# Optimization experiments

Hardware: AMD Instinct MI355X
Metric: run time of the kernel (lower is better)

Reference implementation:

```python
import jax, jax.numpy as jnp
import numpy as np

ALPHA = 1.0
BETA = 1.0
GAMMA = 1.0
WEIGHT_LOSS = 1.0
EPS_DENOM = 1e-20


def setup_inputs() -> dict:
    key = jax.random.key(0)
    k1, k2 = jax.random.split(key)
    B, P, C = 128, 256, 1000
    classification_head_weight = jax.random.normal(k1, (C, P), dtype=jnp.float32)
    similarity_score = jax.random.uniform(k2, (B, P), dtype=jnp.float32)
    return {
        "classification_head_weight": classification_head_weight,
        "similarity_score": similarity_score,
    }


def reference(classification_head_weight, similarity_score):
    # importance[b, p, c] = similarity_score[b, p] * classification_head_weight[c, p]
    imp = jnp.einsum('bp,cp->bpc', similarity_score, classification_head_weight)
    B, P, C = imp.shape
    imp_sq = imp * imp

    # norm over p (dim=1) -> [B, C]; sum over c -> [B]
    norm_over_p = jnp.sqrt(jnp.sum(imp_sq, axis=1))      # [B, C]
    term_a = jnp.sum(norm_over_p, axis=1) ** 2           # [B]
    # norm over c (dim=2) -> [B, P]; sum over p -> [B]
    norm_over_c = jnp.sqrt(jnp.sum(imp_sq, axis=2))      # [B, P]
    term_b = jnp.sum(norm_over_c, axis=1) ** 2           # [B]
    # frobenius norm over (p, c) per batch
    fro_sq = jnp.sum(imp_sq, axis=(1, 2))                # [B]
    fro = jnp.sqrt(fro_sq)                               # [B]

    sparsity = (ALPHA * term_a + BETA * term_b) / (fro_sq + EPS_DENOM)
    sparsity = sparsity / (P * C) ** 0.5
    sparsity = sparsity + GAMMA * fro
    loss = jnp.mean(sparsity)
    return WEIGHT_LOSS * loss
```

## Files before the change

### kernel.cpp

```cpp
#include <hip/hip_runtime.h>
#include <math.h>

#define BB 128
#define PP 256
#define CC 1000

#define NMAIN 504
#define NPREP 16
#define NCT   63

#define OFF_W  0
#define OFF_SQ 4096

__global__ __launch_bounds__(256) void k_one(const float* __restrict__ W,
                                             const float* __restrict__ S,
                                             float* __restrict__ wsf,
                                             float* __restrict__ out) {
    int bid = blockIdx.x;
    int t = threadIdx.x;

    if (bid < NMAIN) {
        __shared__ float s2s[16][260];
        __shared__ float red_sq[16][17];

        int bt = bid & 7;
        int ct = bid >> 3;
        int b0 = bt * 16;
        int c0 = ct * 16;

#pragma unroll
        for (int i = 0; i < 16; ++i) {
            int idx = t + 256 * i;
            int row = idx >> 8, col = idx & 255;
            float s = S[(b0 + row) * PP + col];
            s2s[row][col] = s * s;
        }
        __syncthreads();

        int bl = t & 15;
        int cl = t >> 4;
        int c = c0 + cl;

        float acc = 0.f;
        if (c < CC) {
            const float4* w4 = (const float4*)(W + c * PP);
#pragma unroll 4
            for (int p = 0; p < 64; ++p) {
                float4 w = w4[p];
                float4 s2 = *(const float4*)&s2s[bl][p * 4];
                acc += s2.x * (w.x * w.x);
                acc += s2.y * (w.y * w.y);
                acc += s2.z * (w.z * w.z);
                acc += s2.w * (w.w * w.w);
            }
        }
        float sq = (c < CC) ? sqrtf(acc) : 0.f;

        red_sq[cl][bl] = sq;
        __syncthreads();

        if (t < 16) {
            float ssum = 0.f;
#pragma unroll
            for (int j = 0; j < 16; ++j) ssum += red_sq[j][t];
            __hip_atomic_store(&wsf[OFF_SQ + ct * BB + b0 + t], ssum,
                               __ATOMIC_RELAXED, __HIP_MEMORY_SCOPE_AGENT);
        }
        return;
    }

    if (bid < NMAIN + NPREP) {
        int k = bid - NMAIN;
        int c_lo = k * 64;
        int c_hi = min(CC, c_lo + 64);
        float acc = 0.f;
        for (int c = c_lo; c < c_hi; ++c) {
            float w = W[c * PP + t];
            acc += w * w;
        }
        __hip_atomic_store(&wsf[OFF_W + k * 256 + t], acc,
                           __ATOMIC_RELAXED, __HIP_MEMORY_SCOPE_AGENT);
        return;
    }

    __shared__ float sw[PP];
    __shared__ float wsqs[PP];
    __shared__ float red[BB];

    {
        float v[NPREP];
        bool ok;
        do {
            ok = true;
#pragma unroll
            for (int k = 0; k < NPREP; ++k)
                v[k] = __hip_atomic_load(&wsf[OFF_W + k * 256 + t],
                                         __ATOMIC_RELAXED,
                                         __HIP_MEMORY_SCOPE_AGENT);
#pragma unroll
            for (int k = 0; k < NPREP; ++k) ok &= (v[k] >= 0.f);
            if (!ok) __builtin_amdgcn_s_sleep(1);
        } while (!ok);
        float a = 0.f;
#pragma unroll
        for (int k = 0; k < NPREP; ++k) a += v[k];
        wsqs[t] = a;
        sw[t] = sqrtf(a);
    }
    __syncthreads();

    if (t < BB) {
        int b = t;
        float tb = 0.f, fsq = 0.f;
        const float4* s4 = (const float4*)(S + b * PP);
#pragma unroll 8
        for (int p = 0; p < PP / 4; ++p) {
            float4 s = s4[p];
            tb  += fabsf(s.x) * sw[p * 4 + 0];
            tb  += fabsf(s.y) * sw[p * 4 + 1];
            tb  += fabsf(s.z) * sw[p * 4 + 2];
            tb  += fabsf(s.w) * sw[p * 4 + 3];
            fsq += s.x * s.x * wsqs[p * 4 + 0];
            fsq += s.y * s.y * wsqs[p * 4 + 1];
            fsq += s.z * s.z * wsqs[p * 4 + 2];
            fsq += s.w * s.w * wsqs[p * 4 + 3];
        }

        float ta = 0.f;
        for (int chunk = 0; chunk < 4; ++chunk) {
            int base = chunk * 16;
            int n = (chunk < 3) ? 16 : (NCT - 48);
            float v[16];
            bool ok;
            do {
                ok = true;
#pragma unroll
                for (int j = 0; j < 16; ++j) {
                    int ct = base + j;
                    if (ct < NCT)
                        v[j] = __hip_atomic_load(&wsf[OFF_SQ + ct * BB + b],
                                                 __ATOMIC_RELAXED,
                                                 __HIP_MEMORY_SCOPE_AGENT);
                    else
                        v[j] = 0.f;
                }
#pragma unroll
                for (int j = 0; j < 16; ++j) ok &= (v[j] >= 0.f);
                if (!ok) __builtin_amdgcn_s_sleep(1);
            } while (!ok);
            (void)n;
#pragma unroll
            for (int j = 0; j < 16; ++j) ta += v[j];
        }

        float inv_scale = 1.0f / sqrtf((float)(PP * CC));
        float sparsity = (ta * ta + tb * tb) / (fsq + 1e-20f);
        sparsity *= inv_scale;
        sparsity += sqrtf(fsq);
        red[b] = sparsity;
    }
    __syncthreads();
    if (t == 0) {
        float sum = 0.f;
        for (int i = 0; i < BB; ++i) sum += red[i];
        out[0] = sum / (float)BB;
    }
}

extern "C" void kernel_launch(void* const* d_in, const int* in_sizes, int n_in,
                              void* d_out, int out_size, void* d_ws, size_t ws_size,
                              hipStream_t stream) {
    const float* W = (const float*)d_in[0];
    const float* S = (const float*)d_in[1];
    float* out = (float*)d_out;
    float* ws = (float*)d_ws;

    hipLaunchKernelGGL(k_one, dim3(NMAIN + NPREP + 1), dim3(256), 0, stream,
                       W, S, ws, out);
}
```

Before: 16.50 us.

## Restructure single-kernel loss into fewer 512-thread blocks with split final reduction

Reduces the main grid from 504 to 128 blocks of 512 threads, each thread computing two class rows and reading S directly from global memory instead of staging squared S in shared memory. The W column-norm prep uses 8 blocks split in halves, and the final block spreads the per-batch dot products and flag polling across 512 threads, finishing with a shuffle reduction. This is meant to cut launch, staging and serial tail cost. In exchange each thread does more work and there is less parallelism per class tile. The readiness checks now use strict >0, which relies on the workspace being pre-filled with a negative sentinel and on the partial sums being positive.

Result: slower. 27.64 us (+67.6%).

```diff
diff --git a/kernel.cpp b/kernel.cpp
--- a/kernel.cpp
+++ b/kernel.cpp
@@ -5,165 +5,177 @@
 #define PP 256
 #define CC 1000
 
-#define NMAIN 504
-#define NPREP 16
-#define NCT   63
+#define NMAINB 128
+#define NPREPB 8
+#define NBLK   (NMAINB + NPREPB + 1)
 
 #define OFF_W  0
-#define OFF_SQ 4096
+#define OFF_SQ 2048
 
-__global__ __launch_bounds__(256) void k_one(const float* __restrict__ W,
+__global__ __launch_bounds__(512) void k_one(const float* __restrict__ W,
                                              const float* __restrict__ S,
                                              float* __restrict__ wsf,
                                              float* __restrict__ out) {
     int bid = blockIdx.x;
     int t = threadIdx.x;
 
-    if (bid < NMAIN) {
-        __shared__ float s2s[16][260];
-        __shared__ float red_sq[16][17];
+    if (bid < NMAINB) {
+        __shared__ float red_sq[32][17];
 
         int bt = bid & 7;
-        int ct = bid >> 3;
+        int cg = bid >> 3;
         int b0 = bt * 16;
-        int c0 = ct * 16;
-
-#pragma unroll
-        for (int i = 0; i < 16; ++i) {
-            int idx = t + 256 * i;
-            int row = idx >> 8, col = idx & 255;
-            float s = S[(b0 + row) * PP + col];
-            s2s[row][col] = s * s;
-        }
-        __syncthreads();
+        int c0 = cg * 64;
 
         int bl = t & 15;
         int cl = t >> 4;
-        int c = c0 + cl;
+        int b = b0 + bl;
+        int cA = c0 + cl;
+        int cB = c0 + cl + 32;
+        bool vA = (cA < CC), vB = (cB < CC);
 
-        float acc = 0.f;
-        if (c < CC) {
-            const float4* w4 = (const float4*)(W + c * PP);
+        const float4* s4  = (const float4*)(S + b * PP);
+        const float4* wA4 = (const float4*)(W + (vA ? cA : 0) * PP);
+        const float4* wB4 = (const float4*)(W + (vB ? cB : 0) * PP);
+
+        float accA = 0.f, accB = 0.f;
 #pragma unroll 4
-            for (int p = 0; p < 64; ++p) {
-                float4 w = w4[p];
-                float4 s2 = *(const float4*)&s2s[bl][p * 4];
-                acc += s2.x * (w.x * w.x);
-                acc += s2.y * (w.y * w.y);
-                acc += s2.z * (w.z * w.z);
-                acc += s2.w * (w.w * w.w);
-            }
+        for (int p4 = 0; p4 < 64; ++p4) {
+            float4 s = s4[p4];
+            float4 a = wA4[p4];
+            float4 c = wB4[p4];
+            float x;
+            x = s.x * a.x; accA = fmaf(x, x, accA);
+            x = s.y * a.y; accA = fmaf(x, x, accA);
+            x = s.z * a.z; accA = fmaf(x, x, accA);
+            x = s.w * a.w; accA = fmaf(x, x, accA);
+            x = s.x * c.x; accB = fmaf(x, x, accB);
+            x = s.y * c.y; accB = fmaf(x, x, accB);
+            x = s.z * c.z; accB = fmaf(x, x, accB);
+            x = s.w * c.w; accB = fmaf(x, x, accB);
         }
-        float sq = (c < CC) ? sqrtf(acc) : 0.f;
+        float part = (vA ? sqrtf(accA) : 0.f) + (vB ? sqrtf(accB) : 0.f);
 
-        red_sq[cl][bl] = sq;
+        red_sq[cl][bl] = part;
         __syncthreads();
 
         if (t < 16) {
             float ssum = 0.f;
 #pragma unroll
-            for (int j = 0; j < 16; ++j) ssum += red_sq[j][t];
-            __hip_atomic_store(&wsf[OFF_SQ + ct * BB + b0 + t], ssum,
+            for (int j = 0; j < 32; ++j) ssum += red_sq[j][t];
+            __hip_atomic_store(&wsf[OFF_SQ + cg * BB + b0 + t], ssum,
                                __ATOMIC_RELAXED, __HIP_MEMORY_SCOPE_AGENT);
         }
         return;
     }
 
-    if (bid < NMAIN + NPREP) {
-        int k = bid - NMAIN;
-        int c_lo = k * 64;
-        int c_hi = min(CC, c_lo + 64);
+    if (bid < NMAINB + NPREPB) {
+        __shared__ float redw[2][256];
+        int k = bid - NMAINB;
+        int p = t & 255;
+        int half = t >> 8;
+        int base = k * 125 + (half ? 63 : 0);
+        int n = half ? 62 : 63;
         float acc = 0.f;
-        for (int c = c_lo; c < c_hi; ++c) {
-            float w = W[c * PP + t];
-            acc += w * w;
+#pragma unroll 4
+        for (int i = 0; i < n; ++i) {
+            float w = W[(base + i) * PP + p];
+            acc = fmaf(w, w, acc);
         }
-        __hip_atomic_store(&wsf[OFF_W + k * 256 + t], acc,
-                           __ATOMIC_RELAXED, __HIP_MEMORY_SCOPE_AGENT);
+        redw[half][p] = acc;
+        __syncthreads();
+        if (t < 256)
+            __hip_atomic_store(&wsf[OFF_W + k * 256 + t],
+                               redw[0][t] + redw[1][t],
+                               __ATOMIC_RELAXED, __HIP_MEMORY_SCOPE_AGENT);
         return;
     }
 
     __shared__ float sw[PP];
     __shared__ float wsqs[PP];
+    __shared__ float rta[4][BB];
+    __shared__ float rtb[4][BB];
+    __shared__ float rfq[4][BB];
     __shared__ float red[BB];
 
-    {
-        float v[NPREP];
+    if (t < 256) {
+        float v[NPREPB];
         bool ok;
         do {
             ok = true;
 #pragma unroll
-            for (int k = 0; k < NPREP; ++k)
+            for (int k = 0; k < NPREPB; ++k)
                 v[k] = __hip_atomic_load(&wsf[OFF_W + k * 256 + t],
                                          __ATOMIC_RELAXED,
                                          __HIP_MEMORY_SCOPE_AGENT);
 #pragma unroll
-            for (int k = 0; k < NPREP; ++k) ok &= (v[k] >= 0.f);
+            for (int k = 0; k < NPREPB; ++k) ok &= (v[k] > 0.f);
             if (!ok) __builtin_amdgcn_s_sleep(1);
         } while (!ok);
         float a = 0.f;
 #pragma unroll
-        for (int k = 0; k < NPREP; ++k) a += v[k];
+        for (int k = 0; k < NPREPB; ++k) a += v[k];
         wsqs[t] = a;
         sw[t] = sqrtf(a);
     }
     __syncthreads();
 
-    if (t < BB) {
-        int b = t;
-        float tb = 0.f, fsq = 0.f;
+    int b = t & 127;
+    int q = t >> 7;
+    {
+        float tb = 0.f, fq = 0.f;
         const float4* s4 = (const float4*)(S + b * PP);
-#pragma unroll 8
-        for (int p = 0; p < PP / 4; ++p) {
-            float4 s = s4[p];
-            tb  += fabsf(s.x) * sw[p * 4 + 0];
-            tb  += fabsf(s.y) * sw[p * 4 + 1];
-            tb  += fabsf(s.z) * sw[p * 4 + 2];
-            tb  += fabsf(s.w) * sw[p * 4 + 3];
-            fsq += s.x * s.x * wsqs[p * 4 + 0];
-            fsq += s.y * s.y * wsqs[p * 4 + 1];
-            fsq += s.z * s.z * wsqs[p * 4 + 2];
-            fsq += s.w * s.w * wsqs[p * 4 + 3];
+#pragma unroll
+        for (int p4 = q * 16; p4 < q * 16 + 16; ++p4) {
+            float4 s = s4[p4];
+            tb += fabsf(s.x) * sw[4 * p4 + 0];
+            tb += fabsf(s.y) * sw[4 * p4 + 1];
+            tb += fabsf(s.z) * sw[4 * p4 + 2];
+            tb += fabsf(s.w) * sw[4 * p4 + 3];
+            fq = fmaf(s.x * s.x, wsqs[4 * p4 + 0], fq);
+            fq = fmaf(s.y * s.y, wsqs[4 * p4 + 1], fq);
+            fq = fmaf(s.z * s.z, wsqs[4 * p4 + 2], fq);
+            fq = fmaf(s.w * s.w, wsqs[4 * p4 + 3], fq);
         }
+        rtb[q][b] = tb;
+        rfq[q][b] = fq;
+    }
 
-        float ta = 0.f;
-        for (int chunk = 0; chunk < 4; ++chunk) {
-            int base = chunk * 16;
-            int n = (chunk < 3) ? 16 : (NCT - 48);
-            float v[16];
-            bool ok;
-            do {
-                ok = true;
+    {
+        float v[4];
+        bool ok;
+        do {
+            ok = true;
 #pragma unroll
-                for (int j = 0; j < 16; ++j) {
-                    int ct = base + j;
-                    if (ct < NCT)
-                        v[j] = __hip_atomic_load(&wsf[OFF_SQ + ct * BB + b],
-                                                 __ATOMIC_RELAXED,
-                                                 __HIP_MEMORY_SCOPE_AGENT);
-                    else
-                        v[j] = 0.f;
-                }
+            for (int j = 0; j < 4; ++j)
+                v[j] = __hip_atomic_load(&wsf[OFF_SQ + (q * 4 + j) * BB + b],
+                                         __ATOMIC_RELAXED,
+                                         __HIP_MEMORY_SCOPE_AGENT);
 #pragma unroll
-                for (int j = 0; j < 16; ++j) ok &= (v[j] >= 0.f);
-                if (!ok) __builtin_amdgcn_s_sleep(1);
-            } while (!ok);
-            (void)n;
-#pragma unroll
-            for (int j = 0; j < 16; ++j) ta += v[j];
-        }
-
-        float inv_scale = 1.0f / sqrtf((float)(PP * CC));
-        float sparsity = (ta * ta + tb * tb) / (fsq + 1e-20f);
-        sparsity *= inv_scale;
-        sparsity += sqrtf(fsq);
-        red[b] = sparsity;
+            for (int j = 0; j < 4; ++j) ok &= (v[j] > 0.f);
+            if (!ok) __builtin_amdgcn_s_sleep(1);
+        } while (!ok);
+        rta[q][b] = v[0] + v[1] + v[2] + v[3];
     }
     __syncthreads();
-    if (t == 0) {
-        float sum = 0.f;
-        for (int i = 0; i < BB; ++i) sum += red[i];
-        out[0] = sum / (float)BB;
+
+    if (t < BB) {
+        float TA = rta[0][t] + rta[1][t] + rta[2][t] + rta[3][t];
+        float TB = rtb[0][t] + rtb[1][t] + rtb[2][t] + rtb[3][t];
+        float FQ = rfq[0][t] + rfq[1][t] + rfq[2][t] + rfq[3][t];
+        float inv_scale = 1.0f / sqrtf((float)(PP * CC));
+        float sp = (TA * TA + TB * TB) / (FQ + 1e-20f);
+        sp = sp * inv_scale + sqrtf(FQ);
+        red[t] = sp;
+    }
+    __syncthreads();
+
+    if (t < 64) {
+        float v = red[t] + red[t + 64];
+#pragma unroll
+        for (int off = 32; off > 0; off >>= 1)
+            v += __shfl_down(v, off);
+        if (t == 0) out[0] = v / (float)BB;
     }
 }
 
@@ -175,6 +187,5 @@
     float* out = (float*)d_out;
     float* ws = (float*)d_ws;
 
-    hipLaunchKernelGGL(k_one, dim3(NMAIN + NPREP + 1), dim3(256), 0, stream,
-                       W, S, ws, out);
+    hipLaunchKernelGGL(k_one, dim3(NBLK), dim3(512), 0, stream, W, S, ws, out);
 }
```
